# Performance work log

Hardware: AMD Instinct MI355X
Metric: run time of the kernel (lower is better)

## Reference

```python
import jax, jax.numpy as jnp
import numpy as np

L, B, E, H = 512, 32, 1024, 16
NEG = -1e9  # finite stand-in for masked_fill(-inf); avoids NaNs if a row were fully masked


def setup_inputs() -> dict:
    key = jax.random.key(0)
    ks = jax.random.split(key, 6)
    s_in = (2.0 / (3 * E + E)) ** 0.5   # xavier-ish scale for in_proj
    s_out = (2.0 / (E + E)) ** 0.5
    return {
        "query": jax.random.normal(ks[0], (L, B, E), jnp.float32),
        "key": jax.random.normal(ks[1], (L, B, E), jnp.float32),
        "value": jax.random.normal(ks[2], (L, B, E), jnp.float32),
        "attn_mask": jax.random.randint(ks[3], (B, L, L), 0, 2).astype(jnp.bool_),
        "in_proj_weight": jax.random.normal(ks[4], (3 * E, E), jnp.float32) * s_in,
        "in_proj_bias": jnp.zeros((3 * E,), jnp.float32),
        "out_proj_weight": jax.random.normal(ks[5], (E, E), jnp.float32) * s_out,
        "out_proj_bias": jnp.zeros((E,), jnp.float32),
        "num_heads": H,
    }


def reference(query, key, value, attn_mask, in_proj_weight, in_proj_bias,
              out_proj_weight, out_proj_bias, num_heads):
    Lq, Bz, Em = query.shape
    hd = Em // num_heads
    Wq, Wk, Wv = jnp.split(in_proj_weight, 3, axis=0)
    bq, bk, bv = jnp.split(in_proj_bias, 3, axis=0)
    # in-projection: x @ W^T + b  (torch F.linear convention)
    q = query @ Wq.T + bq
    k = key @ Wk.T + bk
    v = value @ Wv.T + bv
    # [L, B, E] -> [B*H, L, hd], batch-major (b*H + h) per torch view semantics
    def split_heads(x):
        return x.reshape(x.shape[0], Bz * num_heads, hd).transpose(1, 0, 2)
    q, k, v = split_heads(q), split_heads(k), split_heads(v)
    q = q / jnp.sqrt(jnp.asarray(hd, q.dtype))
    # scores: [B*H, Lq, Lk]
    attn = jnp.einsum('bqd,bkd->bqk', q, k)
    # mask broadcast to heads: [B, L, L] -> [B*H, L, L] with index b*H + h
    mask_mh = jnp.repeat(attn_mask, num_heads, axis=0)
    # original: scatter zeros where masked, then masked_fill(-inf) inside
    # multi_head_positional_attention; net effect = mask -> -inf before softmax
    attn = jnp.where(mask_mh, NEG, attn)
    p = jax.nn.softmax(attn, axis=-1)
    out = jnp.einsum('bqk,bkd->bqd', p, v)        # [B*H, Lq, hd]
    out = out.transpose(1, 0, 2).reshape(Lq, Bz, Em)
    out = out @ out_proj_weight.T + out_proj_bias  # [L, B, E]
    return out
```

## Files before the change

kernel.cpp:

```cpp
#include <hip/hip_runtime.h>
#include <hip/hip_bf16.h>
#include <stdint.h>

#define LSEQ 512
#define BATCH 32
#define EMB 1024
#define NHEAD 16
#define HDIM 64
#define TOK (LSEQ*BATCH)
#define BHTOT (BATCH*NHEAD)

typedef __attribute__((ext_vector_type(8))) short short8;
typedef __attribute__((ext_vector_type(4))) short short4v;
typedef __attribute__((ext_vector_type(4))) float f32x4;

__device__ __forceinline__ short f2bf(float f) {
  __hip_bfloat16 h = __float2bfloat16(f);
  union { __hip_bfloat16 h; short s; } u; u.h = h;
  return u.s;
}

__device__ __forceinline__ short8 cvt8(f32x4 x0, f32x4 x1) {
  short8 o;
  o[0] = f2bf(x0[0]); o[1] = f2bf(x0[1]); o[2] = f2bf(x0[2]); o[3] = f2bf(x0[3]);
  o[4] = f2bf(x1[0]); o[5] = f2bf(x1[1]); o[6] = f2bf(x1[2]); o[7] = f2bf(x1[3]);
  return o;
}

#if defined(__has_builtin)
#if __has_builtin(__builtin_amdgcn_global_load_lds)
#define HAVE_GLL 1
#endif
#endif

__device__ __forceinline__ void gload_lds16(const void* g, void* l) {
#ifdef HAVE_GLL
  __builtin_amdgcn_global_load_lds((const __attribute__((address_space(1))) void*)g,
                                   (__attribute__((address_space(3))) void*)l, 16, 0, 0);
#else
  *(short8*)l = *(const short8*)g;
#endif
}

__global__ void cast_weights(const float* __restrict__ W, const float* __restrict__ Wo,
                             const float* __restrict__ bias,
                             short* __restrict__ Wb, short* __restrict__ Wob,
                             float* __restrict__ biasp)
{
  int i = blockIdx.x * 256 + threadIdx.x;
  if (i < 786432) {
    f32x4 v = ((const f32x4*)W)[i];
    int row = i >> 8;
    float s = (row < 1024) ? 0.125f : 1.0f;
    short4v o;
    o[0] = f2bf(v[0]*s); o[1] = f2bf(v[1]*s); o[2] = f2bf(v[2]*s); o[3] = f2bf(v[3]*s);
    ((short4v*)Wb)[i] = o;
  } else {
    int j = i - 786432;
    f32x4 v = ((const f32x4*)Wo)[j];
    short4v o;
    o[0] = f2bf(v[0]); o[1] = f2bf(v[1]); o[2] = f2bf(v[2]); o[3] = f2bf(v[3]);
    ((short4v*)Wob)[j] = o;
  }
  if (i < 768) {
    f32x4 v = ((const f32x4*)bias)[i];
    float s = (i < 256) ? 0.125f : 1.0f;
    f32x4 o = {v[0]*s, v[1]*s, v[2]*s, v[3]*s};
    ((f32x4*)biasp)[i] = o;
  }
}

__global__ void maskbits_kernel(const int* __restrict__ mask, uint32_t* __restrict__ mb)
{
  int w = (blockIdx.x * 256 + threadIdx.x) >> 6;
  int lane = threadIdx.x & 63;
  const int* src = mask + ((size_t)w << 9);
  uint32_t* dst = mb + w * 16;
  #pragma unroll
  for (int c = 0; c < 8; ++c) {
    int v = src[c * 64 + lane];
    unsigned long long m = __ballot(v != 0);
    if (lane == 0) dst[c*2]     = (uint32_t)m;
    if (lane == 1) dst[c*2 + 1] = (uint32_t)(m >> 32);
  }
}

__launch_bounds__(256, 4)
__global__ void proj_gemm(const float* __restrict__ Aq, const float* __restrict__ Ak,
                          const float* __restrict__ Av, const short* __restrict__ W,
                          const float* __restrict__ biasp,
                          short* __restrict__ qh, short* __restrict__ kh,
                          short* __restrict__ vh)
{
  int z = blockIdx.z;
  const float* A = (z == 0) ? Aq : (z == 1) ? Ak : Av;
  short* C       = (z == 0) ? qh : (z == 1) ? kh : vh;
  const short* B = W + (size_t)z * 1024 * 1024;
  const float* bp = biasp + z * 1024;

  int flat = blockIdx.y * 8 + blockIdx.x;
  int X = flat & 7, s = flat >> 3;
  int m0 = (X * 16 + (s >> 3)) * 128;
  int n0 = (s & 7) * 128;

  __shared__ alignas(16) short As[2][128 * 32];
  __shared__ alignas(16) short Bs[2][128 * 32];

  const int tid = threadIdx.x, lane = tid & 63;
  const int w = tid >> 6;
  const int wm = (w >> 1) * 64, wn = (w & 1) * 64;
  const int l15 = lane & 15, l4 = lane >> 4;

  const float* aSrc[2];
  const short* bSrc[2];
  int aDst[2], bDst[2];
  #pragma unroll
  for (int jj = 0; jj < 2; ++jj) {
    int ch = tid + jj * 256;
    int row = ch >> 2, cl = ch & 3;
    int cs = cl ^ ((row >> 1) & 3);
    aSrc[jj] = A + (size_t)(m0 + row) * 1024 + cl * 8;
    bSrc[jj] = B + (size_t)(n0 + row) * 1024 + cs * 8;
    aDst[jj] = row * 32 + cs * 8;
    bDst[jj] = ch * 8;
  }

  f32x4 acc[4][4];
  #pragma unroll
  for (int mi = 0; mi < 4; ++mi)
    #pragma unroll
    for (int ni = 0; ni < 4; ++ni) acc[mi][ni] = f32x4{0.f, 0.f, 0.f, 0.f};

  #pragma unroll
  for (int jj = 0; jj < 2; ++jj) {
    f32x4 x0 = *(const f32x4*)(aSrc[jj]);
    f32x4 x1 = *(const f32x4*)(aSrc[jj] + 4);
    *(short8*)&As[0][aDst[jj]] = cvt8(x0, x1);
    gload_lds16(bSrc[jj], &Bs[0][bDst[jj]]);
  }
  __syncthreads();

  int cur = 0;
  for (int k0 = 0; k0 < 1024; k0 += 32) {
    const int nxt = cur ^ 1;
    const bool has_next = (k0 + 32) < 1024;

    f32x4 xa0[2], xa1[2];
    if (has_next) {
      #pragma unroll
      for (int jj = 0; jj < 2; ++jj) {
        xa0[jj] = *(const f32x4*)(aSrc[jj] + k0 + 32);
        xa1[jj] = *(const f32x4*)(aSrc[jj] + k0 + 36);
        gload_lds16(bSrc[jj] + k0 + 32, &Bs[nxt][bDst[jj]]);
      }
    }

    short8 af[4], bfr[4];
    #pragma unroll
    for (int mi = 0; mi < 4; ++mi) {
      int row = wm + mi * 16 + l15;
      int cs = l4 ^ ((row >> 1) & 3);
      af[mi] = *(const short8*)&As[cur][row * 32 + cs * 8];
    }
    #pragma unroll
    for (int ni = 0; ni < 4; ++ni) {
      int row = wn + ni * 16 + l15;
      int cs = l4 ^ ((row >> 1) & 3);
      bfr[ni] = *(const short8*)&Bs[cur][row * 32 + cs * 8];
    }

    #pragma unroll
    for (int mi = 0; mi < 4; ++mi)
      #pragma unroll
      for (int ni = 0; ni < 4; ++ni)
        acc[mi][ni] = __builtin_amdgcn_mfma_f32_16x16x32_bf16(af[mi], bfr[ni], acc[mi][ni], 0, 0, 0);

    if (has_next) {
      #pragma unroll
      for (int jj = 0; jj < 2; ++jj)
        *(short8*)&As[nxt][aDst[jj]] = cvt8(xa0[jj], xa1[jj]);
    }

    __syncthreads();
    cur = nxt;
  }

  #pragma unroll
  for (int ni = 0; ni < 4; ++ni) {
    int gcol = n0 + wn + ni * 16 + l15;
    float bv = bp[gcol];
    int h = gcol >> 6, d = gcol & 63;
    #pragma unroll
    for (int mi = 0; mi < 4; ++mi) {
      int growb = m0 + wm + mi * 16 + l4 * 4;
      #pragma unroll
      for (int r = 0; r < 4; ++r) {
        int grow = growb + r;
        int lsq = grow >> 5, bb = grow & 31;
        C[((size_t)((bb * NHEAD + h) * LSEQ + lsq)) * HDIM + d] = f2bf(acc[mi][ni][r] + bv);
      }
    }
  }
}

__launch_bounds__(256, 2)
__global__ void attn_kernel(const short* __restrict__ qh, const short* __restrict__ kh,
                            const short* __restrict__ vh, const uint32_t* __restrict__ mb,
                            short* __restrict__ ao)
{
  int flat = blockIdx.y * 8 + blockIdx.x;
  int X = flat & 7, s = flat >> 3;
  int bh = X * 64 + (s >> 3);
  int qblk = s & 7;
  int b = bh >> 4, h = bh & 15;
  int q0 = qblk * 64;

  const int tid = threadIdx.x, lane = tid & 63, w = tid >> 6;
  const int l15 = lane & 15, l4 = lane >> 4;

  __shared__ alignas(16) short Ks[64 * 64];
  __shared__ alignas(16) short Vt[64 * 72];
  __shared__ alignas(16) short Ps[4 * 16 * 72];
  __shared__ uint32_t Mw[64 * 2];

  const size_t bhoff = (size_t)bh * (LSEQ * HDIM);

  short8 aq[2];
  {
    int qrow = q0 + w * 16 + l15;
    const short* qp = qh + bhoff + (size_t)qrow * HDIM + l4 * 8;
    aq[0] = *(const short8*)qp;
    aq[1] = *(const short8*)(qp + 32);
  }

  f32x4 oacc[4];
  #pragma unroll
  for (int n = 0; n < 4; ++n) oacc[n] = f32x4{0.f, 0.f, 0.f, 0.f};
  float m_i[4], l_i[4];
  #pragma unroll
  for (int r = 0; r < 4; ++r) { m_i[r] = -1e30f; l_i[r] = 0.f; }

  for (int kt = 0; kt < 8; ++kt) {
    __syncthreads();
    #pragma unroll
    for (int jj = 0; jj < 2; ++jj) {
      int ch = tid + jj * 256;
      int row = ch >> 3, cl = ch & 7;
      int cg = cl ^ (row & 7);
      const short* g = kh + bhoff + (size_t)(kt * 64 + row) * HDIM + cg * 8;
      gload_lds16(g, &Ks[ch * 8]);
    }
    #pragma unroll
    for (int jj = 0; jj < 2; ++jj) {
      int c = tid + jj * 256;
      int kv = c & 63, d0 = (c >> 6) * 8;
      const short* g = vh + bhoff + (size_t)(kt * 64 + kv) * HDIM + d0;
      short8 vv = *(const short8*)g;
      #pragma unroll
      for (int j = 0; j < 8; ++j) Vt[(d0 + j) * 72 + kv] = vv[j];
    }
    if (tid < 128) {
      int qr = tid >> 1, wd = tid & 1;
      Mw[qr * 2 + wd] = mb[((size_t)b * LSEQ + q0 + qr) * 16 + kt * 2 + wd];
    }
    __syncthreads();

    f32x4 sa[4];
    #pragma unroll
    for (int n = 0; n < 4; ++n) sa[n] = f32x4{0.f, 0.f, 0.f, 0.f};
    #pragma unroll
    for (int ss = 0; ss < 2; ++ss) {
      #pragma unroll
      for (int n = 0; n < 4; ++n) {
        int row = n * 16 + l15;
        int cs = (ss * 4 + l4) ^ (row & 7);
        short8 bk = *(const short8*)&Ks[row * 64 + cs * 8];
        sa[n] = __builtin_amdgcn_mfma_f32_16x16x32_bf16(aq[ss], bk, sa[n], 0, 0, 0);
      }
    }

    #pragma unroll
    for (int r = 0; r < 4; ++r) {
      int qr = w * 16 + l4 * 4 + r;
      uint32_t mlo = Mw[qr * 2], mhi = Mw[qr * 2 + 1];
      float sv[4];
      #pragma unroll
      for (int n = 0; n < 4; ++n) {
        int cc = n * 16 + l15;
        uint32_t bit = ((cc < 32 ? (mlo >> cc) : (mhi >> (cc - 32))) & 1u);
        sv[n] = bit ? -1e9f : sa[n][r];
      }
      float rmax = fmaxf(fmaxf(sv[0], sv[1]), fmaxf(sv[2], sv[3]));
      #pragma unroll
      for (int off = 1; off < 16; off <<= 1) rmax = fmaxf(rmax, __shfl_xor(rmax, off, 64));
      float mn = fmaxf(m_i[r], rmax);
      float sc = __expf(m_i[r] - mn);
      float p0 = __expf(sv[0] - mn), p1 = __expf(sv[1] - mn);
      float p2 = __expf(sv[2] - mn), p3 = __expf(sv[3] - mn);
      float rs = p0 + p1 + p2 + p3;
      #pragma unroll
      for (int off = 1; off < 16; off <<= 1) rs += __shfl_xor(rs, off, 64);
      l_i[r] = l_i[r] * sc + rs;
      m_i[r] = mn;
      #pragma unroll
      for (int n = 0; n < 4; ++n) oacc[n][r] *= sc;
      short* pp = &Ps[w * 1152 + (l4 * 4 + r) * 72];
      pp[0 * 16 + l15] = f2bf(p0);
      pp[1 * 16 + l15] = f2bf(p1);
      pp[2 * 16 + l15] = f2bf(p2);
      pp[3 * 16 + l15] = f2bf(p3);
    }

    #pragma unroll
    for (int ss = 0; ss < 2; ++ss) {
      short8 pa = *(const short8*)&Ps[w * 1152 + l15 * 72 + ss * 32 + l4 * 8];
      #pragma unroll
      for (int n = 0; n < 4; ++n) {
        short8 bv = *(const short8*)&Vt[(n * 16 + l15) * 72 + ss * 32 + l4 * 8];
        oacc[n] = __builtin_amdgcn_mfma_f32_16x16x32_bf16(pa, bv, oacc[n], 0, 0, 0);
      }
    }
  }

  #pragma unroll
  for (int r = 0; r < 4; ++r) {
    float inv = 1.0f / l_i[r];
    int qrow = q0 + w * 16 + l4 * 4 + r;
    size_t tbase = ((size_t)qrow * BATCH + b) * EMB + h * HDIM;
    #pragma unroll
    for (int n = 0; n < 4; ++n)
      ao[tbase + n * 16 + l15] = f2bf(oacc[n][r] * inv);
  }
}

__launch_bounds__(256, 4)
__global__ void out_gemm(const short* __restrict__ Ab, const short* __restrict__ W,
                         const float* __restrict__ bo, float* __restrict__ out)
{
  int flat = blockIdx.y * 8 + blockIdx.x;
  int X = flat & 7, s = flat >> 3;
  int m0 = (X * 16 + (s >> 3)) * 128;
  int n0 = (s & 7) * 128;

  __shared__ alignas(16) short As[2][128 * 32];
  __shared__ alignas(16) short Bs[2][128 * 32];

  const int tid = threadIdx.x, lane = tid & 63;
  const int w = tid >> 6;
  const int wm = (w >> 1) * 64, wn = (w & 1) * 64;
  const int l15 = lane & 15, l4 = lane >> 4;

  const short* aSrc[2];
  const short* bSrc[2];
  int sDst[2];
  #pragma unroll
  for (int jj = 0; jj < 2; ++jj) {
    int ch = tid + jj * 256;
    int row = ch >> 2, cl = ch & 3;
    int cs = cl ^ ((row >> 1) & 3);
    aSrc[jj] = Ab + (size_t)(m0 + row) * 1024 + cs * 8;
    bSrc[jj] = W + (size_t)(n0 + row) * 1024 + cs * 8;
    sDst[jj] = ch * 8;
  }

  f32x4 acc[4][4];
  #pragma unroll
  for (int mi = 0; mi < 4; ++mi)
    #pragma unroll
    for (int ni = 0; ni < 4; ++ni) acc[mi][ni] = f32x4{0.f, 0.f, 0.f, 0.f};

  #pragma unroll
  for (int jj = 0; jj < 2; ++jj) {
    gload_lds16(aSrc[jj], &As[0][sDst[jj]]);
    gload_lds16(bSrc[jj], &Bs[0][sDst[jj]]);
  }
  __syncthreads();

  int cur = 0;
  for (int k0 = 0; k0 < 1024; k0 += 32) {
    const int nxt = cur ^ 1;
    const bool has_next = (k0 + 32) < 1024;

    if (has_next) {
      #pragma unroll
      for (int jj = 0; jj < 2; ++jj) {
        gload_lds16(aSrc[jj] + k0 + 32, &As[nxt][sDst[jj]]);
        gload_lds16(bSrc[jj] + k0 + 32, &Bs[nxt][sDst[jj]]);
      }
    }

    short8 af[4], bfr[4];
    #pragma unroll
    for (int mi = 0; mi < 4; ++mi) {
      int row = wm + mi * 16 + l15;
      int cs = l4 ^ ((row >> 1) & 3);
      af[mi] = *(const short8*)&As[cur][row * 32 + cs * 8];
    }
    #pragma unroll
    for (int ni = 0; ni < 4; ++ni) {
      int row = wn + ni * 16 + l15;
      int cs = l4 ^ ((row >> 1) & 3);
      bfr[ni] = *(const short8*)&Bs[cur][row * 32 + cs * 8];
    }
    #pragma unroll
    for (int mi = 0; mi < 4; ++mi)
      #pragma unroll
      for (int ni = 0; ni < 4; ++ni)
        acc[mi][ni] = __builtin_amdgcn_mfma_f32_16x16x32_bf16(af[mi], bfr[ni], acc[mi][ni], 0, 0, 0);

    __syncthreads();
    cur = nxt;
  }

  #pragma unroll
  for (int ni = 0; ni < 4; ++ni) {
    int gcol = n0 + wn + ni * 16 + l15;
    float bv = bo[gcol];
    #pragma unroll
    for (int mi = 0; mi < 4; ++mi) {
      int growb = m0 + wm + mi * 16 + l4 * 4;
      #pragma unroll
      for (int r = 0; r < 4; ++r)
        out[(size_t)(growb + r) * 1024 + gcol] = acc[mi][ni][r] + bv;
    }
  }
}

extern "C" void kernel_launch(void* const* d_in, const int* in_sizes, int n_in,
                              void* d_out, int out_size, void* d_ws, size_t ws_size,
                              hipStream_t stream) {
  const float* q_in = (const float*)d_in[0];
  const float* k_in = (const float*)d_in[1];
  const float* v_in = (const float*)d_in[2];
  const int*   mask = (const int*)d_in[3];
  const float* Wp   = (const float*)d_in[4];
  const float* bp   = (const float*)d_in[5];
  const float* Wo   = (const float*)d_in[6];
  const float* bo   = (const float*)d_in[7];

  char* ws = (char*)d_ws;
  short* Wb    = (short*)ws;    ws += (size_t)3072 * 1024 * 2;
  short* Wob   = (short*)ws;    ws += (size_t)1024 * 1024 * 2;
  float* biasp = (float*)ws;    ws += (size_t)3072 * 4;
  short* qh    = (short*)ws;    ws += (size_t)TOK * EMB * 2;
  short* kh    = (short*)ws;    ws += (size_t)TOK * EMB * 2;
  short* vh    = (short*)ws;    ws += (size_t)TOK * EMB * 2;
  short* ao    = (short*)ws;    ws += (size_t)TOK * EMB * 2;
  uint32_t* mb = (uint32_t*)ws; ws += (size_t)BATCH * LSEQ * 16 * 4;

  cast_weights<<<4096, 256, 0, stream>>>(Wp, Wo, bp, Wb, Wob, biasp);
  maskbits_kernel<<<4096, 256, 0, stream>>>(mask, mb);
  proj_gemm<<<dim3(8, 128, 3), 256, 0, stream>>>(q_in, k_in, v_in, Wb, biasp, qh, kh, vh);
  attn_kernel<<<dim3(8, 512), 256, 0, stream>>>(qh, kh, vh, mb, ao);
  out_gemm<<<dim3(8, 128), 256, 0, stream>>>(ao, Wob, bo, (float*)d_out);
}
```

Before: 365.7 us.

## Restructure projection GEMMs into two-stage-ahead prefetch with explicit waitcnt barriers

Both the input-projection and output-projection GEMMs now run a manually unrolled ping-pong loop. Global loads for the tile two steps ahead are issued right after the fragment reads, and explicit s_waitcnt vmcnt/lgkmcnt plus s_barrier replace __syncthreads. This keeps two tiles of loads in flight so memory latency overlaps the MFMA work, at the cost of more live registers. To make room, proj_gemm's launch bound drops from 4 to 3 waves per SIMD. Correctness now depends on the hand-counted vmcnt values matching the number of outstanding loads.

```diff
diff --git a/kernel.cpp b/kernel.cpp
--- a/kernel.cpp
+++ b/kernel.cpp
@@ -41,6 +41,12 @@
   *(short8*)l = *(const short8*)g;
 #endif
 }
+
+#define WAIT_VM6  do { asm volatile("s_waitcnt vmcnt(6)" ::: "memory"); __builtin_amdgcn_sched_barrier(0); } while (0)
+#define WAIT_VM4  do { asm volatile("s_waitcnt vmcnt(4)" ::: "memory"); __builtin_amdgcn_sched_barrier(0); } while (0)
+#define WAIT_VM0  do { asm volatile("s_waitcnt vmcnt(0)" ::: "memory"); __builtin_amdgcn_sched_barrier(0); } while (0)
+#define WAIT_LGKM0 do { asm volatile("s_waitcnt lgkmcnt(0)" ::: "memory"); __builtin_amdgcn_sched_barrier(0); } while (0)
+#define BAR() __builtin_amdgcn_s_barrier()
 
 __global__ void cast_weights(const float* __restrict__ W, const float* __restrict__ Wo,
                              const float* __restrict__ bias,
@@ -85,7 +91,29 @@
   }
 }
 
-__launch_bounds__(256, 4)
+#define FRAG_READ(AsX, BsX)                                           \
+    short8 af[4], bfr[4];                                             \
+    _Pragma("unroll")                                                 \
+    for (int mi = 0; mi < 4; ++mi) {                                  \
+      int row = wm + mi * 16 + l15;                                   \
+      int cs = l4 ^ ((row >> 1) & 3);                                 \
+      af[mi] = *(const short8*)&AsX[row * 32 + cs * 8];               \
+    }                                                                 \
+    _Pragma("unroll")                                                 \
+    for (int ni = 0; ni < 4; ++ni) {                                  \
+      int row = wn + ni * 16 + l15;                                   \
+      int cs = l4 ^ ((row >> 1) & 3);                                 \
+      bfr[ni] = *(const short8*)&BsX[row * 32 + cs * 8];              \
+    }
+
+#define DO_MFMA()                                                     \
+    _Pragma("unroll")                                                 \
+    for (int mi = 0; mi < 4; ++mi)                                    \
+      _Pragma("unroll")                                               \
+      for (int ni = 0; ni < 4; ++ni)                                  \
+        acc[mi][ni] = __builtin_amdgcn_mfma_f32_16x16x32_bf16(af[mi], bfr[ni], acc[mi][ni], 0, 0, 0)
+
+__launch_bounds__(256, 3)
 __global__ void proj_gemm(const float* __restrict__ Aq, const float* __restrict__ Ak,
                           const float* __restrict__ Av, const short* __restrict__ W,
                           const float* __restrict__ biasp,
@@ -99,12 +127,14 @@
   const float* bp = biasp + z * 1024;
 
   int flat = blockIdx.y * 8 + blockIdx.x;
-  int X = flat & 7, s = flat >> 3;
-  int m0 = (X * 16 + (s >> 3)) * 128;
-  int n0 = (s & 7) * 128;
-
-  __shared__ alignas(16) short As[2][128 * 32];
-  __shared__ alignas(16) short Bs[2][128 * 32];
+  int X = flat & 7, s0 = flat >> 3;
+  int m0 = (X * 16 + (s0 >> 3)) * 128;
+  int n0 = (s0 & 7) * 128;
+
+  __shared__ alignas(16) short As0[128 * 32];
+  __shared__ alignas(16) short As1[128 * 32];
+  __shared__ alignas(16) short Bs0[128 * 32];
+  __shared__ alignas(16) short Bs1[128 * 32];
 
   const int tid = threadIdx.x, lane = tid & 63;
   const int w = tid >> 6;
@@ -131,58 +161,81 @@
     #pragma unroll
     for (int ni = 0; ni < 4; ++ni) acc[mi][ni] = f32x4{0.f, 0.f, 0.f, 0.f};
 
+  f32x4 ea0[2], ea1[2];
+  f32x4 oa0[2], oa1[2];
+
   #pragma unroll
   for (int jj = 0; jj < 2; ++jj) {
-    f32x4 x0 = *(const f32x4*)(aSrc[jj]);
-    f32x4 x1 = *(const f32x4*)(aSrc[jj] + 4);
-    *(short8*)&As[0][aDst[jj]] = cvt8(x0, x1);
-    gload_lds16(bSrc[jj], &Bs[0][bDst[jj]]);
-  }
-  __syncthreads();
-
-  int cur = 0;
-  for (int k0 = 0; k0 < 1024; k0 += 32) {
-    const int nxt = cur ^ 1;
-    const bool has_next = (k0 + 32) < 1024;
-
-    f32x4 xa0[2], xa1[2];
-    if (has_next) {
+    gload_lds16(bSrc[jj], &Bs0[bDst[jj]]);
+    ea0[jj] = *(const f32x4*)(aSrc[jj]);
+    ea1[jj] = *(const f32x4*)(aSrc[jj] + 4);
+  }
+  #pragma unroll
+  for (int jj = 0; jj < 2; ++jj)
+    *(short8*)&As0[aDst[jj]] = cvt8(ea0[jj], ea1[jj]);
+  WAIT_VM0;
+  #pragma unroll
+  for (int jj = 0; jj < 2; ++jj) {
+    gload_lds16(bSrc[jj] + 32, &Bs1[bDst[jj]]);
+    oa0[jj] = *(const f32x4*)(aSrc[jj] + 32);
+    oa1[jj] = *(const f32x4*)(aSrc[jj] + 36);
+  }
+  WAIT_LGKM0;
+  BAR();
+
+  for (int i = 0; i < 15; ++i) {
+    const int s = 2 * i;
+    {
+      FRAG_READ(As0, Bs0);
+      WAIT_LGKM0;
+      BAR();
       #pragma unroll
       for (int jj = 0; jj < 2; ++jj) {
-        xa0[jj] = *(const f32x4*)(aSrc[jj] + k0 + 32);
-        xa1[jj] = *(const f32x4*)(aSrc[jj] + k0 + 36);
-        gload_lds16(bSrc[jj] + k0 + 32, &Bs[nxt][bDst[jj]]);
-      }
-    }
-
-    short8 af[4], bfr[4];
-    #pragma unroll
-    for (int mi = 0; mi < 4; ++mi) {
-      int row = wm + mi * 16 + l15;
-      int cs = l4 ^ ((row >> 1) & 3);
-      af[mi] = *(const short8*)&As[cur][row * 32 + cs * 8];
-    }
-    #pragma unroll
-    for (int ni = 0; ni < 4; ++ni) {
-      int row = wn + ni * 16 + l15;
-      int cs = l4 ^ ((row >> 1) & 3);
-      bfr[ni] = *(const short8*)&Bs[cur][row * 32 + cs * 8];
-    }
-
-    #pragma unroll
-    for (int mi = 0; mi < 4; ++mi)
-      #pragma unroll
-      for (int ni = 0; ni < 4; ++ni)
-        acc[mi][ni] = __builtin_amdgcn_mfma_f32_16x16x32_bf16(af[mi], bfr[ni], acc[mi][ni], 0, 0, 0);
-
-    if (has_next) {
+        gload_lds16(bSrc[jj] + (s + 2) * 32, &Bs0[bDst[jj]]);
+        ea0[jj] = *(const f32x4*)(aSrc[jj] + (s + 2) * 32);
+        ea1[jj] = *(const f32x4*)(aSrc[jj] + (s + 2) * 32 + 4);
+      }
+      DO_MFMA();
       #pragma unroll
       for (int jj = 0; jj < 2; ++jj)
-        *(short8*)&As[nxt][aDst[jj]] = cvt8(xa0[jj], xa1[jj]);
-    }
-
-    __syncthreads();
-    cur = nxt;
+        *(short8*)&As1[aDst[jj]] = cvt8(oa0[jj], oa1[jj]);
+      WAIT_VM6;
+      WAIT_LGKM0;
+      BAR();
+    }
+    {
+      FRAG_READ(As1, Bs1);
+      WAIT_LGKM0;
+      BAR();
+      #pragma unroll
+      for (int jj = 0; jj < 2; ++jj) {
+        gload_lds16(bSrc[jj] + (s + 3) * 32, &Bs1[bDst[jj]]);
+        oa0[jj] = *(const f32x4*)(aSrc[jj] + (s + 3) * 32);
+        oa1[jj] = *(const f32x4*)(aSrc[jj] + (s + 3) * 32 + 4);
+      }
+      DO_MFMA();
+      #pragma unroll
+      for (int jj = 0; jj < 2; ++jj)
+        *(short8*)&As0[aDst[jj]] = cvt8(ea0[jj], ea1[jj]);
+      WAIT_VM6;
+      WAIT_LGKM0;
+      BAR();
+    }
+  }
+
+  {
+    FRAG_READ(As0, Bs0);
+    DO_MFMA();
+    #pragma unroll
+    for (int jj = 0; jj < 2; ++jj)
+      *(short8*)&As1[aDst[jj]] = cvt8(oa0[jj], oa1[jj]);
+    WAIT_VM0;
+    WAIT_LGKM0;
+    BAR();
+  }
+  {
+    FRAG_READ(As1, Bs1);
+    DO_MFMA();
   }
 
   #pragma unroll
@@ -338,12 +391,14 @@
                          const float* __restrict__ bo, float* __restrict__ out)
 {
   int flat = blockIdx.y * 8 + blockIdx.x;
-  int X = flat & 7, s = flat >> 3;
-  int m0 = (X * 16 + (s >> 3)) * 128;
-  int n0 = (s & 7) * 128;
-
-  __shared__ alignas(16) short As[2][128 * 32];
-  __shared__ alignas(16) short Bs[2][128 * 32];
+  int X = flat & 7, s0 = flat >> 3;
+  int m0 = (X * 16 + (s0 >> 3)) * 128;
+  int n0 = (s0 & 7) * 128;
+
+  __shared__ alignas(16) short As0[128 * 32];
+  __shared__ alignas(16) short As1[128 * 32];
+  __shared__ alignas(16) short Bs0[128 * 32];
+  __shared__ alignas(16) short Bs1[128 * 32];
 
   const int tid = threadIdx.x, lane = tid & 63;
   const int w = tid >> 6;
@@ -371,45 +426,56 @@
 
   #pragma unroll
   for (int jj = 0; jj < 2; ++jj) {
-    gload_lds16(aSrc[jj], &As[0][sDst[jj]]);
-    gload_lds16(bSrc[jj], &Bs[0][sDst[jj]]);
-  }
-  __syncthreads();
-
-  int cur = 0;
-  for (int k0 = 0; k0 < 1024; k0 += 32) {
-    const int nxt = cur ^ 1;
-    const bool has_next = (k0 + 32) < 1024;
-
-    if (has_next) {
+    gload_lds16(aSrc[jj], &As0[sDst[jj]]);
+    gload_lds16(bSrc[jj], &Bs0[sDst[jj]]);
+  }
+  #pragma unroll
+  for (int jj = 0; jj < 2; ++jj) {
+    gload_lds16(aSrc[jj] + 32, &As1[sDst[jj]]);
+    gload_lds16(bSrc[jj] + 32, &Bs1[sDst[jj]]);
+  }
+  WAIT_VM4;
+  BAR();
+
+  for (int i = 0; i < 15; ++i) {
+    const int s = 2 * i;
+    {
+      FRAG_READ(As0, Bs0);
+      WAIT_LGKM0;
+      BAR();
       #pragma unroll
       for (int jj = 0; jj < 2; ++jj) {
-        gload_lds16(aSrc[jj] + k0 + 32, &As[nxt][sDst[jj]]);
-        gload_lds16(bSrc[jj] + k0 + 32, &Bs[nxt][sDst[jj]]);
-      }
-    }
-
-    short8 af[4], bfr[4];
-    #pragma unroll
-    for (int mi = 0; mi < 4; ++mi) {
-      int row = wm + mi * 16 + l15;
-      int cs = l4 ^ ((row >> 1) & 3);
-      af[mi] = *(const short8*)&As[cur][row * 32 + cs * 8];
-    }
-    #pragma unroll
-    for (int ni = 0; ni < 4; ++ni) {
-      int row = wn + ni * 16 + l15;
-      int cs = l4 ^ ((row >> 1) & 3);
-      bfr[ni] = *(const short8*)&Bs[cur][row * 32 + cs * 8];
-    }
-    #pragma unroll
-    for (int mi = 0; mi < 4; ++mi)
-      #pragma unroll
-      for (int ni = 0; ni < 4; ++ni)
-        acc[mi][ni] = __builtin_amdgcn_mfma_f32_16x16x32_bf16(af[mi], bfr[ni], acc[mi][ni], 0, 0, 0);
-
-    __syncthreads();
-    cur = nxt;
+        gload_lds16(aSrc[jj] + (s + 2) * 32, &As0[sDst[jj]]);
+        gload_lds16(bSrc[jj] + (s + 2) * 32, &Bs0[sDst[jj]]);
+      }
+      DO_MFMA();
+      WAIT_VM4;
+      BAR();
+    }
+    {
+      FRAG_READ(As1, Bs1);
+      WAIT_LGKM0;
+      BAR();
+      #pragma unroll
+      for (int jj = 0; jj < 2; ++jj) {
+        gload_lds16(aSrc[jj] + (s + 3) * 32, &As1[sDst[jj]]);
+        gload_lds16(bSrc[jj] + (s + 3) * 32, &Bs1[sDst[jj]]);
+      }
+      DO_MFMA();
+      WAIT_VM4;
+      BAR();
+    }
+  }
+
+  {
+    FRAG_READ(As0, Bs0);
+    DO_MFMA();
+    WAIT_VM0;
+    BAR();
+  }
+  {
+    FRAG_READ(As1, Bs1);
+    DO_MFMA();
   }
 
   #pragma unroll
```

Result: no change. 362.4 us (-0.9%).
